# Optimization experiments

Hardware: AMD Instinct MI355X
Metric: run time of the kernel (lower is better)

The kernel has to match this reference:

```python
import jax, jax.numpy as jnp
import numpy as np

INPUT_SIZE = 512
HIDDEN_SIZE = 256
OUTPUT_SIZE = 128
T = 2048
B = 64


def setup_inputs() -> dict:
    key = jax.random.key(0)
    ks = jax.random.split(key, 7)
    s_ih = 1.0 / np.sqrt(HIDDEN_SIZE)
    inputs = jax.random.normal(ks[0], (T, B, INPUT_SIZE), dtype=jnp.float32)
    # PyTorch LSTMCell params: weight_ih [4H, I], weight_hh [4H, H], biases [4H]
    W_ih = jax.random.uniform(ks[1], (4 * HIDDEN_SIZE, INPUT_SIZE), minval=-s_ih, maxval=s_ih, dtype=jnp.float32)
    W_hh = jax.random.uniform(ks[2], (4 * HIDDEN_SIZE, HIDDEN_SIZE), minval=-s_ih, maxval=s_ih, dtype=jnp.float32)
    b_ih = jax.random.uniform(ks[3], (4 * HIDDEN_SIZE,), minval=-s_ih, maxval=s_ih, dtype=jnp.float32)
    b_hh = jax.random.uniform(ks[4], (4 * HIDDEN_SIZE,), minval=-s_ih, maxval=s_ih, dtype=jnp.float32)
    s_fc = 1.0 / np.sqrt(HIDDEN_SIZE)
    W_fc = jax.random.uniform(ks[5], (OUTPUT_SIZE, HIDDEN_SIZE), minval=-s_fc, maxval=s_fc, dtype=jnp.float32)
    b_fc = jax.random.uniform(ks[6], (OUTPUT_SIZE,), minval=-s_fc, maxval=s_fc, dtype=jnp.float32)
    return {"inputs": inputs, "W_ih": W_ih, "W_hh": W_hh, "b_ih": b_ih,
            "b_hh": b_hh, "W_fc": W_fc, "b_fc": b_fc}


def reference(inputs, W_ih, W_hh, b_ih, b_hh, W_fc, b_fc):
    # Eval-mode forward: dropout is identity (training=False) and noise is
    # only injected when training, so the math is a plain LSTMCell recurrence
    # followed by a per-step Linear.
    Bsz = inputs.shape[1]
    H = W_hh.shape[1]

    def step(carry, x):
        h, c = carry
        gates = x @ W_ih.T + b_ih + h @ W_hh.T + b_hh  # [B, 4H]
        i, f, g, o = jnp.split(gates, 4, axis=-1)       # PyTorch gate order
        c = jax.nn.sigmoid(f) * c + jax.nn.sigmoid(i) * jnp.tanh(g)
        h = jax.nn.sigmoid(o) * jnp.tanh(c)
        return (h, c), h

    h0 = jnp.zeros((Bsz, H), dtype=inputs.dtype)
    c0 = jnp.zeros((Bsz, H), dtype=inputs.dtype)
    _, hs = jax.lax.scan(step, (h0, c0), inputs)        # [T, B, H]
    return hs @ W_fc.T + b_fc                           # [T, B, output_size]
```

## Files before the change

### kernel.cpp

```cpp
#include <hip/hip_runtime.h>

#define T_STEPS 2048
#define BATCH   64
#define ISZ     512
#define HSZ     256
#define G4      1024
#define OSZ     128

typedef __attribute__((ext_vector_type(8))) short short8;
typedef __attribute__((ext_vector_type(4))) float f32x4;

__device__ __forceinline__ unsigned short f32_to_bf16(float x) {
  unsigned int u = __float_as_uint(x);
  unsigned int r = (u + 0x7FFFu + ((u >> 16) & 1u)) >> 16;
  return (unsigned short)r;
}
__device__ __forceinline__ float bf16_to_f32(unsigned short s) {
  return __uint_as_float(((unsigned int)s) << 16);
}
__device__ __forceinline__ float tanh_fast(float x) {
  return 1.f - 2.f / (__expf(2.f * x) + 1.f);
}

__global__ void split_bf16_kernel(const float* __restrict__ src,
                                  short* __restrict__ hi, short* __restrict__ lo,
                                  long n) {
  long i = ((long)blockIdx.x * blockDim.x + threadIdx.x) * 4;
  if (i >= n) return;
  float4 v = *(const float4*)(src + i);
  float xs[4] = {v.x, v.y, v.z, v.w};
  short h[4], l[4];
#pragma unroll
  for (int j = 0; j < 4; ++j) {
    unsigned short hb = f32_to_bf16(xs[j]);
    float hf = bf16_to_f32(hb);
    unsigned short lb = f32_to_bf16(xs[j] - hf);
    h[j] = (short)hb; l[j] = (short)lb;
  }
  *(short4*)(hi + i) = make_short4(h[0], h[1], h[2], h[3]);
  *(short4*)(lo + i) = make_short4(l[0], l[1], l[2], l[3]);
}

__global__ void zero_u32_kernel(unsigned int* __restrict__ p, int n) {
  int i = blockIdx.x * blockDim.x + threadIdx.x;
  if (i < n) p[i] = 0u;
}

__global__ __launch_bounds__(256) void gemm_bf16x3(
    const short* __restrict__ Ahi, const short* __restrict__ Alo,
    const short* __restrict__ Bhi, const short* __restrict__ Blo,
    const float* __restrict__ bias1, const float* __restrict__ bias2,
    float* __restrict__ C, int N, int K) {
  const int tid  = threadIdx.x;
  const int lane = tid & 63;
  const int wv   = tid >> 6;
  const int lrow = lane & 15;
  const int kgrp = lane >> 4;
  const int m0 = blockIdx.x * 64 + wv * 16;
  const int n0 = blockIdx.y * 64;

  const short* pah = Ahi + (size_t)(m0 + lrow) * K + kgrp * 8;
  const short* pal = Alo + (size_t)(m0 + lrow) * K + kgrp * 8;
  const short* pbh = Bhi + (size_t)(n0 + lrow) * K + kgrp * 8;
  const short* pbl = Blo + (size_t)(n0 + lrow) * K + kgrp * 8;
  const size_t cs = (size_t)16 * K;

  f32x4 acc0 = {0.f, 0.f, 0.f, 0.f};
  f32x4 acc1 = acc0, acc2 = acc0, acc3 = acc0;

  for (int kb = 0; kb < K; kb += 32) {
    short8 ah  = *(const short8*)(pah + kb);
    short8 al  = *(const short8*)(pal + kb);
    short8 b0h = *(const short8*)(pbh + kb);
    short8 b0l = *(const short8*)(pbl + kb);
    short8 b1h = *(const short8*)(pbh + cs + kb);
    short8 b1l = *(const short8*)(pbl + cs + kb);
    short8 b2h = *(const short8*)(pbh + 2 * cs + kb);
    short8 b2l = *(const short8*)(pbl + 2 * cs + kb);
    short8 b3h = *(const short8*)(pbh + 3 * cs + kb);
    short8 b3l = *(const short8*)(pbl + 3 * cs + kb);

    acc0 = __builtin_amdgcn_mfma_f32_16x16x32_bf16(ah, b0h, acc0, 0, 0, 0);
    acc1 = __builtin_amdgcn_mfma_f32_16x16x32_bf16(ah, b1h, acc1, 0, 0, 0);
    acc2 = __builtin_amdgcn_mfma_f32_16x16x32_bf16(ah, b2h, acc2, 0, 0, 0);
    acc3 = __builtin_amdgcn_mfma_f32_16x16x32_bf16(ah, b3h, acc3, 0, 0, 0);
    acc0 = __builtin_amdgcn_mfma_f32_16x16x32_bf16(al, b0h, acc0, 0, 0, 0);
    acc1 = __builtin_amdgcn_mfma_f32_16x16x32_bf16(al, b1h, acc1, 0, 0, 0);
    acc2 = __builtin_amdgcn_mfma_f32_16x16x32_bf16(al, b2h, acc2, 0, 0, 0);
    acc3 = __builtin_amdgcn_mfma_f32_16x16x32_bf16(al, b3h, acc3, 0, 0, 0);
    acc0 = __builtin_amdgcn_mfma_f32_16x16x32_bf16(ah, b0l, acc0, 0, 0, 0);
    acc1 = __builtin_amdgcn_mfma_f32_16x16x32_bf16(ah, b1l, acc1, 0, 0, 0);
    acc2 = __builtin_amdgcn_mfma_f32_16x16x32_bf16(ah, b2l, acc2, 0, 0, 0);
    acc3 = __builtin_amdgcn_mfma_f32_16x16x32_bf16(ah, b3l, acc3, 0, 0, 0);
  }

  f32x4 accs[4] = {acc0, acc1, acc2, acc3};
#pragma unroll
  for (int c = 0; c < 4; ++c) {
    const int col = n0 + c * 16 + lrow;
    float bs = bias1[col];
    if (bias2) bs += bias2[col];
#pragma unroll
    for (int r = 0; r < 4; ++r) {
      const int row = m0 + kgrp * 4 + r;
      C[(size_t)row * N + col] = accs[c][r] + bs;
    }
  }
}

__global__ __launch_bounds__(256, 1) void lstm_rec(
    const float* __restrict__ G,
    const float* __restrict__ Whh,
    short* __restrict__ HShi, short* __restrict__ HSlo,
    unsigned long long* __restrict__ hslots,
    float* __restrict__ c_buf,
    int t0, int nsteps) {
  const int tid  = threadIdx.x;
  const int part = blockIdx.x >> 6;
  const int b    = blockIdx.x & 63;
  const int q    = tid >> 6;
  const int l    = tid & 63;
  const int hidx = part * 64 + l;
  const int j    = q * 256 + hidx;

  float w[256];
  {
    const float* wr = Whh + (size_t)j * 256;
#pragma unroll
    for (int k = 0; k < 256; k += 4) {
      float4 v = *(const float4*)(wr + k);
      w[k] = v.x; w[k + 1] = v.y; w[k + 2] = v.z; w[k + 3] = v.w;
    }
  }

  __shared__ float4 h_s4[64];
  float* h_s = (float*)h_s4;
  __shared__ float gate_s[4][64];

  const int ctid = tid - 64;
  const int ridx = (ctid < part * 64) ? ctid : ctid + 64;

  unsigned long long* slot0 = hslots + (size_t)b * HSZ;
  const size_t slot_stride = (size_t)BATCH * HSZ;

  if (t0 == 0) {
    if (tid < 64) h_s4[tid] = make_float4(0.f, 0.f, 0.f, 0.f);
  } else {
    unsigned long long* ap =
        slot0 + (size_t)((t0 + 1) & 1) * slot_stride + tid;
    unsigned long long v;
    do {
      v = __hip_atomic_load(ap, __ATOMIC_RELAXED, __HIP_MEMORY_SCOPE_AGENT);
    } while ((unsigned)(v >> 32) != (unsigned)t0);
    h_s[tid] = __uint_as_float((unsigned)v);
  }
  float c = 0.f;
  if (q == 0 && t0 > 0) c = c_buf[(size_t)b * HSZ + hidx];

  const float* gbase = G + (size_t)b * G4 + j;
  float gcur = gbase[0];
  __syncthreads();

  for (int t = 0; t < nsteps; ++t) {
    const size_t tn = (t + 1 < nsteps) ? (size_t)(t + 1) : (size_t)(nsteps - 1);
    const float gnx = gbase[tn * (size_t)(BATCH * G4)];

    float a0 = 0.f, a1 = 0.f, a2 = 0.f, a3 = 0.f;
#pragma unroll
    for (int k = 0; k < 256; k += 4) {
      const float4 hv = h_s4[k >> 2];
      a0 = __builtin_fmaf(hv.x, w[k],     a0);
      a1 = __builtin_fmaf(hv.y, w[k + 1], a1);
      a2 = __builtin_fmaf(hv.z, w[k + 2], a2);
      a3 = __builtin_fmaf(hv.w, w[k + 3], a3);
    }
    const float pre = gcur + ((a0 + a1) + (a2 + a3));
    gate_s[q][l] = (q == 2) ? tanh_fast(pre) : 1.f / (1.f + __expf(-pre));
    gcur = gnx;
    __syncthreads();

    const unsigned exp_tag = (unsigned)(t0 + t + 1);
    unsigned long long* slot =
        slot0 + (size_t)((t0 + t) & 1) * slot_stride;

    if (q == 0) {
      const float si = gate_s[0][l];
      const float sf = gate_s[1][l];
      const float tg = gate_s[2][l];
      const float so = gate_s[3][l];
      c = sf * c + si * tg;
      const float h = so * tanh_fast(c);
      const size_t oidx = ((size_t)t * BATCH + b) * HSZ + hidx;
      const unsigned short hb = f32_to_bf16(h);
      const unsigned short lb = f32_to_bf16(h - bf16_to_f32(hb));
      HShi[oidx] = (short)hb;
      HSlo[oidx] = (short)lb;
      h_s[hidx] = h;
      const unsigned long long pk =
          ((unsigned long long)exp_tag << 32) | (unsigned)__float_as_uint(h);
      __hip_atomic_store(slot + hidx, pk, __ATOMIC_RELAXED,
                         __HIP_MEMORY_SCOPE_AGENT);
    } else if (t + 1 < nsteps) {
      unsigned long long v;
      do {
        v = __hip_atomic_load(slot + ridx, __ATOMIC_RELAXED,
                              __HIP_MEMORY_SCOPE_AGENT);
      } while ((unsigned)(v >> 32) != exp_tag);
      h_s[ridx] = __uint_as_float((unsigned)v);
    }
    __syncthreads();
  }

  if (q == 0) c_buf[(size_t)b * HSZ + hidx] = c;
}

extern "C" void kernel_launch(void* const* d_in, const int* in_sizes, int n_in,
                              void* d_out, int out_size, void* d_ws, size_t ws_size,
                              hipStream_t stream) {
  (void)in_sizes; (void)n_in; (void)out_size;
  const float* X   = (const float*)d_in[0];
  const float* Wih = (const float*)d_in[1];
  const float* Whh = (const float*)d_in[2];
  const float* bih = (const float*)d_in[3];
  const float* bhh = (const float*)d_in[4];
  const float* Wfc = (const float*)d_in[5];
  const float* bfc = (const float*)d_in[6];
  float* out = (float*)d_out;

  const size_t fixed =
      2UL * 1048576UL    +
      2UL * 65536UL      +
      262144UL           +
      65536UL;
  const size_t per_step =
      (size_t)BATCH * G4 * 4    +
      2UL * BATCH * ISZ * 2     +
      2UL * BATCH * HSZ * 2    ;
  int CH = 2048;
  while (CH > 16 && fixed + (size_t)CH * per_step > ws_size) CH >>= 1;

  char* p = (char*)d_ws;
  float* Gc    = (float*)p;  p += (size_t)CH * BATCH * G4 * 4;
  short* Xhi   = (short*)p;  p += (size_t)CH * BATCH * ISZ * 2;
  short* Xlo   = (short*)p;  p += (size_t)CH * BATCH * ISZ * 2;
  short* HShi  = (short*)p;  p += (size_t)CH * BATCH * HSZ * 2;
  short* HSlo  = (short*)p;  p += (size_t)CH * BATCH * HSZ * 2;
  short* WihHi = (short*)p;  p += 1048576UL;
  short* WihLo = (short*)p;  p += 1048576UL;
  short* WfcHi = (short*)p;  p += 65536UL;
  short* WfcLo = (short*)p;  p += 65536UL;
  unsigned long long* hslots = (unsigned long long*)p;  p += 262144UL;
  float* c_buf = (float*)p;

  zero_u32_kernel<<<256, 256, 0, stream>>>((unsigned int*)hslots, 65536);
  split_bf16_kernel<<<512, 256, 0, stream>>>(Wih, WihHi, WihLo, 524288L);
  split_bf16_kernel<<<32, 256, 0, stream>>>(Wfc, WfcHi, WfcLo, 32768L);

  const long xchunk_elems = (long)CH * BATCH * ISZ;
  for (int c0 = 0; c0 < T_STEPS; c0 += CH) {
    const float* Xc = X + (size_t)c0 * BATCH * ISZ;
    split_bf16_kernel<<<(int)(xchunk_elems / 1024), 256, 0, stream>>>(
        Xc, Xhi, Xlo, xchunk_elems);
    gemm_bf16x3<<<dim3(CH, 16), 256, 0, stream>>>(Xhi, Xlo, WihHi, WihLo,
                                                  bih, bhh, Gc, 1024, 512);
    lstm_rec<<<256, 256, 0, stream>>>(Gc, Whh, HShi, HSlo, hslots, c_buf,
                                      c0, CH);
    gemm_bf16x3<<<dim3(CH, 2), 256, 0, stream>>>(HShi, HSlo, WfcHi, WfcLo,
                                                 bfc, nullptr,
                                                 out + (size_t)c0 * BATCH * OSZ,
                                                 128, 256);
  }
}
```

Before: 9.335 ms.

## Fuse input-projection GEMM into recurrent LSTM kernel via shared-memory gate ring

Removes the standalone X·W_ih GEMM and its large global gate buffer. Each recurrent block now computes its own input-projection tiles with MFMA, 16 timesteps at a time, into a 64-step shared-memory ring, interleaved with the serial recurrence. The chunked host loop is dropped in favour of one full-sequence split, one fused kernel and one output GEMM. This saves writing and reading the gate buffer in global memory, but adds MFMA work and X/W_ih loads to the latency-critical recurrent loop every 16 steps, where they can stall the cross-block handoff of h.

```diff
diff --git a/kernel.cpp b/kernel.cpp
--- a/kernel.cpp
+++ b/kernel.cpp
@@ -6,6 +6,7 @@
 #define HSZ     256
 #define G4      1024
 #define OSZ     128
+#define RING_D  64
 
 typedef __attribute__((ext_vector_type(8))) short short8;
 typedef __attribute__((ext_vector_type(4))) float f32x4;
@@ -108,13 +109,67 @@
   }
 }
 
-__global__ __launch_bounds__(256, 1) void lstm_rec(
-    const float* __restrict__ G,
+__device__ __forceinline__ void produce_gtile(
+    const short* __restrict__ Xhi, const short* __restrict__ Xlo,
+    const short* __restrict__ WihHi, const short* __restrict__ WihLo,
+    float* __restrict__ ring, int tstep, int b, int q, int part, int lane) {
+  const int m  = lane & 15;
+  const int kg = lane >> 4;
+  const size_t xoff = ((size_t)(tstep + m) * BATCH + b) * ISZ + kg * 8;
+  const short* xh = Xhi + xoff;
+  const short* xl = Xlo + xoff;
+  const size_t roff = (size_t)(q * 256 + part * 64 + m) * ISZ + kg * 8;
+  const short* bh0 = WihHi + roff;
+  const short* bl0 = WihLo + roff;
+  const size_t nts = (size_t)16 * ISZ;
+
+  f32x4 acc0 = {0.f, 0.f, 0.f, 0.f};
+  f32x4 acc1 = acc0, acc2 = acc0, acc3 = acc0;
+
+  for (int kb = 0; kb < ISZ; kb += 32) {
+    short8 ah  = *(const short8*)(xh + kb);
+    short8 al  = *(const short8*)(xl + kb);
+    short8 b0h = *(const short8*)(bh0 + kb);
+    short8 b0l = *(const short8*)(bl0 + kb);
+    short8 b1h = *(const short8*)(bh0 + nts + kb);
+    short8 b1l = *(const short8*)(bl0 + nts + kb);
+    short8 b2h = *(const short8*)(bh0 + 2 * nts + kb);
+    short8 b2l = *(const short8*)(bl0 + 2 * nts + kb);
+    short8 b3h = *(const short8*)(bh0 + 3 * nts + kb);
+    short8 b3l = *(const short8*)(bl0 + 3 * nts + kb);
+
+    acc0 = __builtin_amdgcn_mfma_f32_16x16x32_bf16(ah, b0h, acc0, 0, 0, 0);
+    acc1 = __builtin_amdgcn_mfma_f32_16x16x32_bf16(ah, b1h, acc1, 0, 0, 0);
+    acc2 = __builtin_amdgcn_mfma_f32_16x16x32_bf16(ah, b2h, acc2, 0, 0, 0);
+    acc3 = __builtin_amdgcn_mfma_f32_16x16x32_bf16(ah, b3h, acc3, 0, 0, 0);
+    acc0 = __builtin_amdgcn_mfma_f32_16x16x32_bf16(al, b0h, acc0, 0, 0, 0);
+    acc1 = __builtin_amdgcn_mfma_f32_16x16x32_bf16(al, b1h, acc1, 0, 0, 0);
+    acc2 = __builtin_amdgcn_mfma_f32_16x16x32_bf16(al, b2h, acc2, 0, 0, 0);
+    acc3 = __builtin_amdgcn_mfma_f32_16x16x32_bf16(al, b3h, acc3, 0, 0, 0);
+    acc0 = __builtin_amdgcn_mfma_f32_16x16x32_bf16(ah, b0l, acc0, 0, 0, 0);
+    acc1 = __builtin_amdgcn_mfma_f32_16x16x32_bf16(ah, b1l, acc1, 0, 0, 0);
+    acc2 = __builtin_amdgcn_mfma_f32_16x16x32_bf16(ah, b2l, acc2, 0, 0, 0);
+    acc3 = __builtin_amdgcn_mfma_f32_16x16x32_bf16(ah, b3l, acc3, 0, 0, 0);
+  }
+
+  f32x4 accs[4] = {acc0, acc1, acc2, acc3};
+#pragma unroll
+  for (int nt = 0; nt < 4; ++nt) {
+#pragma unroll
+    for (int r = 0; r < 4; ++r) {
+      const int step = (tstep + kg * 4 + r) & (RING_D - 1);
+      ring[step * 256 + q * 64 + nt * 16 + m] = accs[nt][r];
+    }
+  }
+}
+
+__global__ __launch_bounds__(256, 1) void lstm_fused(
+    const short* __restrict__ Xhi, const short* __restrict__ Xlo,
+    const short* __restrict__ WihHi, const short* __restrict__ WihLo,
+    const float* __restrict__ bih, const float* __restrict__ bhh,
     const float* __restrict__ Whh,
     short* __restrict__ HShi, short* __restrict__ HSlo,
-    unsigned long long* __restrict__ hslots,
-    float* __restrict__ c_buf,
-    int t0, int nsteps) {
+    unsigned long long* __restrict__ hslots) {
   const int tid  = threadIdx.x;
   const int part = blockIdx.x >> 6;
   const int b    = blockIdx.x & 63;
@@ -132,10 +187,12 @@
       w[k] = v.x; w[k + 1] = v.y; w[k + 2] = v.z; w[k + 3] = v.w;
     }
   }
+  const float bias_j = bih[j] + bhh[j];
 
   __shared__ float4 h_s4[64];
   float* h_s = (float*)h_s4;
   __shared__ float gate_s[4][64];
+  __shared__ float ring[RING_D * 256];
 
   const int ctid = tid - 64;
   const int ridx = (ctid < part * 64) ? ctid : ctid + 64;
@@ -143,27 +200,16 @@
   unsigned long long* slot0 = hslots + (size_t)b * HSZ;
   const size_t slot_stride = (size_t)BATCH * HSZ;
 
-  if (t0 == 0) {
-    if (tid < 64) h_s4[tid] = make_float4(0.f, 0.f, 0.f, 0.f);
-  } else {
-    unsigned long long* ap =
-        slot0 + (size_t)((t0 + 1) & 1) * slot_stride + tid;
-    unsigned long long v;
-    do {
-      v = __hip_atomic_load(ap, __ATOMIC_RELAXED, __HIP_MEMORY_SCOPE_AGENT);
-    } while ((unsigned)(v >> 32) != (unsigned)t0);
-    h_s[tid] = __uint_as_float((unsigned)v);
-  }
+  if (tid < 64) h_s4[tid] = make_float4(0.f, 0.f, 0.f, 0.f);
   float c = 0.f;
-  if (q == 0 && t0 > 0) c = c_buf[(size_t)b * HSZ + hidx];
-
-  const float* gbase = G + (size_t)b * G4 + j;
-  float gcur = gbase[0];
+
+  produce_gtile(Xhi, Xlo, WihHi, WihLo, ring, 0,  b, q, part, l);
+  produce_gtile(Xhi, Xlo, WihHi, WihLo, ring, 16, b, q, part, l);
+  produce_gtile(Xhi, Xlo, WihHi, WihLo, ring, 32, b, q, part, l);
   __syncthreads();
 
-  for (int t = 0; t < nsteps; ++t) {
-    const size_t tn = (t + 1 < nsteps) ? (size_t)(t + 1) : (size_t)(nsteps - 1);
-    const float gnx = gbase[tn * (size_t)(BATCH * G4)];
+  for (int t = 0; t < T_STEPS; ++t) {
+    const float gv = ring[(t & (RING_D - 1)) * 256 + q * 64 + l];
 
     float a0 = 0.f, a1 = 0.f, a2 = 0.f, a3 = 0.f;
 #pragma unroll
@@ -174,14 +220,13 @@
       a2 = __builtin_fmaf(hv.z, w[k + 2], a2);
       a3 = __builtin_fmaf(hv.w, w[k + 3], a3);
     }
-    const float pre = gcur + ((a0 + a1) + (a2 + a3));
+    const float pre = (gv + bias_j) + ((a0 + a1) + (a2 + a3));
     gate_s[q][l] = (q == 2) ? tanh_fast(pre) : 1.f / (1.f + __expf(-pre));
-    gcur = gnx;
     __syncthreads();
 
-    const unsigned exp_tag = (unsigned)(t0 + t + 1);
-    unsigned long long* slot =
-        slot0 + (size_t)((t0 + t) & 1) * slot_stride;
+    const unsigned exp_tag = (unsigned)(t + 1);
+    unsigned long long* slot = slot0 + (size_t)(t & 1) * slot_stride;
+    const bool do_prod = ((t & 15) == 0) && (t + RING_D <= T_STEPS);
 
     if (q == 0) {
       const float si = gate_s[0][l];
@@ -200,7 +245,13 @@
           ((unsigned long long)exp_tag << 32) | (unsigned)__float_as_uint(h);
       __hip_atomic_store(slot + hidx, pk, __ATOMIC_RELAXED,
                          __HIP_MEMORY_SCOPE_AGENT);
-    } else if (t + 1 < nsteps) {
+    }
+
+    if (do_prod)
+      produce_gtile(Xhi, Xlo, WihHi, WihLo, ring, t + (RING_D - 16),
+                    b, q, part, l);
+
+    if (q != 0 && t + 1 < T_STEPS) {
       unsigned long long v;
       do {
         v = __hip_atomic_load(slot + ridx, __ATOMIC_RELAXED,
@@ -210,14 +261,12 @@
     }
     __syncthreads();
   }
-
-  if (q == 0) c_buf[(size_t)b * HSZ + hidx] = c;
 }
 
 extern "C" void kernel_launch(void* const* d_in, const int* in_sizes, int n_in,
                               void* d_out, int out_size, void* d_ws, size_t ws_size,
                               hipStream_t stream) {
-  (void)in_sizes; (void)n_in; (void)out_size;
+  (void)in_sizes; (void)n_in; (void)out_size; (void)ws_size;
   const float* X   = (const float*)d_in[0];
   const float* Wih = (const float*)d_in[1];
   const float* Whh = (const float*)d_in[2];
@@ -227,47 +276,26 @@
   const float* bfc = (const float*)d_in[6];
   float* out = (float*)d_out;
 
-  const size_t fixed =
-      2UL * 1048576UL    +
-      2UL * 65536UL      +
-      262144UL           +
-      65536UL;
-  const size_t per_step =
-      (size_t)BATCH * G4 * 4    +
-      2UL * BATCH * ISZ * 2     +
-      2UL * BATCH * HSZ * 2    ;
-  int CH = 2048;
-  while (CH > 16 && fixed + (size_t)CH * per_step > ws_size) CH >>= 1;
-
   char* p = (char*)d_ws;
-  float* Gc    = (float*)p;  p += (size_t)CH * BATCH * G4 * 4;
-  short* Xhi   = (short*)p;  p += (size_t)CH * BATCH * ISZ * 2;
-  short* Xlo   = (short*)p;  p += (size_t)CH * BATCH * ISZ * 2;
-  short* HShi  = (short*)p;  p += (size_t)CH * BATCH * HSZ * 2;
-  short* HSlo  = (short*)p;  p += (size_t)CH * BATCH * HSZ * 2;
+  short* Xhi   = (short*)p;  p += (size_t)T_STEPS * BATCH * ISZ * 2;
+  short* Xlo   = (short*)p;  p += (size_t)T_STEPS * BATCH * ISZ * 2;
+  short* HShi  = (short*)p;  p += (size_t)T_STEPS * BATCH * HSZ * 2;
+  short* HSlo  = (short*)p;  p += (size_t)T_STEPS * BATCH * HSZ * 2;
   short* WihHi = (short*)p;  p += 1048576UL;
   short* WihLo = (short*)p;  p += 1048576UL;
   short* WfcHi = (short*)p;  p += 65536UL;
   short* WfcLo = (short*)p;  p += 65536UL;
-  unsigned long long* hslots = (unsigned long long*)p;  p += 262144UL;
-  float* c_buf = (float*)p;
+  unsigned long long* hslots = (unsigned long long*)p;
 
   zero_u32_kernel<<<256, 256, 0, stream>>>((unsigned int*)hslots, 65536);
   split_bf16_kernel<<<512, 256, 0, stream>>>(Wih, WihHi, WihLo, 524288L);
   split_bf16_kernel<<<32, 256, 0, stream>>>(Wfc, WfcHi, WfcLo, 32768L);
-
-  const long xchunk_elems = (long)CH * BATCH * ISZ;
-  for (int c0 = 0; c0 < T_STEPS; c0 += CH) {
-    const float* Xc = X + (size_t)c0 * BATCH * ISZ;
-    split_bf16_kernel<<<(int)(xchunk_elems / 1024), 256, 0, stream>>>(
-        Xc, Xhi, Xlo, xchunk_elems);
-    gemm_bf16x3<<<dim3(CH, 16), 256, 0, stream>>>(Xhi, Xlo, WihHi, WihLo,
-                                                  bih, bhh, Gc, 1024, 512);
-    lstm_rec<<<256, 256, 0, stream>>>(Gc, Whh, HShi, HSlo, hslots, c_buf,
-                                      c0, CH);
-    gemm_bf16x3<<<dim3(CH, 2), 256, 0, stream>>>(HShi, HSlo, WfcHi, WfcLo,
-                                                 bfc, nullptr,
-                                                 out + (size_t)c0 * BATCH * OSZ,
-                                                 128, 256);
-  }
-}
+  split_bf16_kernel<<<65536, 256, 0, stream>>>(X, Xhi, Xlo, 67108864L);
+
+  lstm_fused<<<256, 256, 0, stream>>>(Xhi, Xlo, WihHi, WihLo, bih, bhh, Whh,
+                                      HShi, HSlo, hslots);
+
+  gemm_bf16x3<<<dim3(T_STEPS, 2), 256, 0, stream>>>(HShi, HSlo, WfcHi, WfcLo,
+                                                    bfc, nullptr, out,
+                                                    128, 256);
+}
```

After: 9.987 ms. 7.0% more time.

## Keep X tile stationary in registers for input-projection GEMM across all N

Applied to the files above, without the earlier changes.

Replaces the 2D-grid input-projection GEMM with a kernel where each block loads its 64-row slab of the split-bf16 X once into registers and loops over all 1024 output columns. This removes the repeated reloading of X across the 16 column blocks. In exchange the grid shrinks by 16x to CH blocks, which may reduce parallelism, and it adds heavy register pressure from 32 short8 values per lane.

```diff
diff --git a/kernel.cpp b/kernel.cpp
--- a/kernel.cpp
+++ b/kernel.cpp
@@ -104,6 +104,77 @@
     for (int r = 0; r < 4; ++r) {
       const int row = m0 + kgrp * 4 + r;
       C[(size_t)row * N + col] = accs[c][r] + bs;
+    }
+  }
+}
+
+__global__ __launch_bounds__(256) void gemm_ih_astat(
+    const short* __restrict__ Ahi, const short* __restrict__ Alo,
+    const short* __restrict__ Bhi, const short* __restrict__ Blo,
+    const float* __restrict__ bias1, const float* __restrict__ bias2,
+    float* __restrict__ C) {
+  const int tid  = threadIdx.x;
+  const int lane = tid & 63;
+  const int wv   = tid >> 6;
+  const int lrow = lane & 15;
+  const int kgrp = lane >> 4;
+  const int m0 = blockIdx.x * 64 + wv * 16;
+  const size_t cs = (size_t)16 * ISZ;
+
+  short8 ah[16], al[16];
+  {
+    const short* pa = Ahi + (size_t)(m0 + lrow) * ISZ + kgrp * 8;
+    const short* pl = Alo + (size_t)(m0 + lrow) * ISZ + kgrp * 8;
+#pragma unroll
+    for (int kb = 0; kb < 16; ++kb) {
+      ah[kb] = *(const short8*)(pa + kb * 32);
+      al[kb] = *(const short8*)(pl + kb * 32);
+    }
+  }
+
+  for (int n0 = 0; n0 < G4; n0 += 64) {
+    const short* pbh = Bhi + (size_t)(n0 + lrow) * ISZ + kgrp * 8;
+    const short* pbl = Blo + (size_t)(n0 + lrow) * ISZ + kgrp * 8;
+
+    f32x4 acc0 = {0.f, 0.f, 0.f, 0.f};
+    f32x4 acc1 = acc0, acc2 = acc0, acc3 = acc0;
+
+#pragma unroll
+    for (int kb = 0; kb < 16; ++kb) {
+      const int ko = kb * 32;
+      short8 b0h = *(const short8*)(pbh + ko);
+      short8 b0l = *(const short8*)(pbl + ko);
+      short8 b1h = *(const short8*)(pbh + cs + ko);
+      short8 b1l = *(const short8*)(pbl + cs + ko);
+      short8 b2h = *(const short8*)(pbh + 2 * cs + ko);
+      short8 b2l = *(const short8*)(pbl + 2 * cs + ko);
+      short8 b3h = *(const short8*)(pbh + 3 * cs + ko);
+      short8 b3l = *(const short8*)(pbl + 3 * cs + ko);
+
+      acc0 = __builtin_amdgcn_mfma_f32_16x16x32_bf16(ah[kb], b0h, acc0, 0, 0, 0);
+      acc1 = __builtin_amdgcn_mfma_f32_16x16x32_bf16(ah[kb], b1h, acc1, 0, 0, 0);
+      acc2 = __builtin_amdgcn_mfma_f32_16x16x32_bf16(ah[kb], b2h, acc2, 0, 0, 0);
+      acc3 = __builtin_amdgcn_mfma_f32_16x16x32_bf16(ah[kb], b3h, acc3, 0, 0, 0);
+      acc0 = __builtin_amdgcn_mfma_f32_16x16x32_bf16(al[kb], b0h, acc0, 0, 0, 0);
+      acc1 = __builtin_amdgcn_mfma_f32_16x16x32_bf16(al[kb], b1h, acc1, 0, 0, 0);
+      acc2 = __builtin_amdgcn_mfma_f32_16x16x32_bf16(al[kb], b2h, acc2, 0, 0, 0);
+      acc3 = __builtin_amdgcn_mfma_f32_16x16x32_bf16(al[kb], b3h, acc3, 0, 0, 0);
+      acc0 = __builtin_amdgcn_mfma_f32_16x16x32_bf16(ah[kb], b0l, acc0, 0, 0, 0);
+      acc1 = __builtin_amdgcn_mfma_f32_16x16x32_bf16(ah[kb], b1l, acc1, 0, 0, 0);
+      acc2 = __builtin_amdgcn_mfma_f32_16x16x32_bf16(ah[kb], b2l, acc2, 0, 0, 0);
+      acc3 = __builtin_amdgcn_mfma_f32_16x16x32_bf16(ah[kb], b3l, acc3, 0, 0, 0);
+    }
+
+    f32x4 accs[4] = {acc0, acc1, acc2, acc3};
+#pragma unroll
+    for (int c = 0; c < 4; ++c) {
+      const int col = n0 + c * 16 + lrow;
+      const float bs = bias1[col] + bias2[col];
+#pragma unroll
+      for (int r = 0; r < 4; ++r) {
+        const int row = m0 + kgrp * 4 + r;
+        C[(size_t)row * G4 + col] = accs[c][r] + bs;
+      }
     }
   }
 }
@@ -261,8 +332,8 @@
     const float* Xc = X + (size_t)c0 * BATCH * ISZ;
     split_bf16_kernel<<<(int)(xchunk_elems / 1024), 256, 0, stream>>>(
         Xc, Xhi, Xlo, xchunk_elems);
-    gemm_bf16x3<<<dim3(CH, 16), 256, 0, stream>>>(Xhi, Xlo, WihHi, WihLo,
-                                                  bih, bhh, Gc, 1024, 512);
+    gemm_ih_astat<<<CH, 256, 0, stream>>>(Xhi, Xlo, WihHi, WihLo,
+                                          bih, bhh, Gc);
     lstm_rec<<<256, 256, 0, stream>>>(Gc, Whh, HShi, HSlo, hslots, c_buf,
                                       c0, CH);
     gemm_bf16x3<<<dim3(CH, 2), 256, 0, stream>>>(HShi, HSlo, WfcHi, WfcLo,
```

Result: faster. 8.740 ms (-6.4%).
